# Optimization experiments

Measured on AMD Instinct MI355X. Metric: run time of the kernel, lower is better.

Reference implementation:

```python
import jax, jax.numpy as jnp
import numpy as np

NUM_LAYERS = 32
HIDDEN_DIM = 2048
RANK = 64
BATCH = 2048


def setup_inputs() -> dict:
    key = jax.random.key(0)
    k_z, k_id, k_u, k_v = jax.random.split(key, 4)
    z = jax.random.normal(k_z, (BATCH, HIDDEN_DIM), dtype=jnp.float32)
    layer_ids = jax.random.randint(k_id, (BATCH,), 0, NUM_LAYERS)
    u = jax.random.normal(k_u, (NUM_LAYERS, HIDDEN_DIM, RANK), dtype=jnp.float32) * 0.01
    v = jax.random.normal(k_v, (NUM_LAYERS, HIDDEN_DIM, RANK), dtype=jnp.float32) * 0.01
    return {"z": z, "layer_ids": layer_ids, "u": u, "v": v}


def reference(z, layer_ids, u, v):
    # Gather per-sample low-rank factors: [B, H, R]
    u_g = u[layer_ids]
    v_g = v[layer_ids]
    # proj = V_l^T z : [B, R]
    proj = jnp.einsum('bhr,bh->br', v_g, z)
    # delta = U_l proj : [B, H]
    delta = jnp.einsum('bhr,br->bh', u_g, proj)
    return z + delta
```

## Files before the change

kernel.cpp:

```cpp
#include <hip/hip_runtime.h>

#define NUM_LAYERS 32
#define HIDDEN 2048
#define RANK 64
#define BATCH 2048
#define CHK 256
#define SCP 2
#define MB 32
#define PPAD 72

typedef __attribute__((ext_vector_type(8))) short bf16x8;
typedef __attribute__((ext_vector_type(4))) float f32x4;

static __device__ __forceinline__ ushort f2bf(float x) {
    unsigned b = __builtin_bit_cast(unsigned, x);
    b += 0x7fffu + ((b >> 16) & 1u);
    return (ushort)(b >> 16);
}
static __device__ __forceinline__ ushort4 pack4(float4 v) {
    ushort4 r; r.x = f2bf(v.x); r.y = f2bf(v.y); r.z = f2bf(v.z); r.w = f2bf(v.w);
    return r;
}
static __device__ __forceinline__ bf16x8 cvt8(float4 a, float4 b) {
    bf16x8 r;
    r[0] = (short)f2bf(a.x); r[1] = (short)f2bf(a.y);
    r[2] = (short)f2bf(a.z); r[3] = (short)f2bf(a.w);
    r[4] = (short)f2bf(b.x); r[5] = (short)f2bf(b.y);
    r[6] = (short)f2bf(b.z); r[7] = (short)f2bf(b.w);
    return r;
}


__global__ __launch_bounds__(256)
void k_setup(const int* __restrict__ ids, float* __restrict__ proj,
             int* __restrict__ counts, int* __restrict__ offsets,
             int* __restrict__ perm)
{
    const int t = threadIdx.x;
    if (blockIdx.x == 0) {
        __shared__ int cnt[NUM_LAYERS];
        __shared__ int off[NUM_LAYERS];
        __shared__ int cur[NUM_LAYERS];
        if (t < NUM_LAYERS) cnt[t] = 0;
        __syncthreads();
        for (int i = t; i < BATCH; i += 256) atomicAdd(&cnt[ids[i]], 1);
        __syncthreads();
        if (t == 0) {
            int a = 0;
            for (int l = 0; l < NUM_LAYERS; ++l) { off[l] = a; a += cnt[l]; }
        }
        __syncthreads();
        if (t < NUM_LAYERS) { cur[t] = 0; counts[t] = cnt[t]; offsets[t] = off[t]; }
        __syncthreads();
        for (int i = t; i < BATCH; i += 256) {
            int l = ids[i];
            int p = off[l] + atomicAdd(&cur[l], 1);
            perm[p] = i;
        }
    } else {
        const int base = (blockIdx.x - 1) * (BATCH * RANK / 64);
        for (int i = t; i < BATCH * RANK / 64; i += 256) proj[base + i] = 0.0f;
    }
}

__global__ __launch_bounds__(256)
void k_proj(const float* __restrict__ z, const float* __restrict__ v,
            const int* __restrict__ counts, const int* __restrict__ offsets,
            const int* __restrict__ perm, float* __restrict__ proj)
{
    const int kc = blockIdx.x, l = blockIdx.y, sc = blockIdx.z;
    const int n = counts[l], o = offsets[l];
    if (sc * MB >= n) return;
    const int t = threadIdx.x;
    const int w = t >> 6, lane = t & 63;
    const int m16 = lane & 15, quad = lane >> 4;
    const int kbase = kc * CHK;

    __shared__ int bidx[MB];

    const float* vp = v + ((size_t)l * HIDDEN + kbase + quad * 8) * RANK
                    + w * 16 + m16;

    for (int base = sc * MB; base < n; base += SCP * MB) {
        const int nb = (n - base < MB) ? (n - base) : MB;
        __syncthreads();
        if (t < MB) bidx[t] = (t < nb) ? perm[o + base + t] : 0;
        __syncthreads();

        const float* zp0 = z + (size_t)bidx[m16] * HIDDEN + kbase + quad * 8;
        const float* zp1 = z + (size_t)bidx[16 + m16] * HIDDEN + kbase + quad * 8;

        f32x4 acc0 = {0.f, 0.f, 0.f, 0.f};
        f32x4 acc1 = {0.f, 0.f, 0.f, 0.f};
        #pragma unroll
        for (int kt = 0; kt < 8; ++kt) {
            float vj[8];
            #pragma unroll
            for (int j = 0; j < 8; ++j) vj[j] = vp[(size_t)(kt * 32 + j) * RANK];
            const bf16x8 bm = cvt8(make_float4(vj[0], vj[1], vj[2], vj[3]),
                                   make_float4(vj[4], vj[5], vj[6], vj[7]));
            const bf16x8 a0 = cvt8(*(const float4*)&zp0[kt * 32],
                                   *(const float4*)&zp0[kt * 32 + 4]);
            const bf16x8 a1 = cvt8(*(const float4*)&zp1[kt * 32],
                                   *(const float4*)&zp1[kt * 32 + 4]);
            acc0 = __builtin_amdgcn_mfma_f32_16x16x32_bf16(a0, bm, acc0, 0, 0, 0);
            acc1 = __builtin_amdgcn_mfma_f32_16x16x32_bf16(a1, bm, acc1, 0, 0, 0);
        }
        #pragma unroll
        for (int reg = 0; reg < 4; ++reg) {
            const int row = quad * 4 + reg;
            if (row < nb)
                atomicAdd(&proj[(size_t)bidx[row] * RANK + w * 16 + m16], acc0[reg]);
            if (16 + row < nb)
                atomicAdd(&proj[(size_t)bidx[16 + row] * RANK + w * 16 + m16], acc1[reg]);
        }
    }
}

__global__ __launch_bounds__(256)
void k_delta(const float* __restrict__ z, const float* __restrict__ u,
             const int* __restrict__ counts, const int* __restrict__ offsets,
             const int* __restrict__ perm, const float* __restrict__ proj,
             float* __restrict__ out)
{
    const int hc = blockIdx.x, l = blockIdx.y, sc = blockIdx.z;
    const int n = counts[l], o = offsets[l];
    if (sc * MB >= n) return;
    const int t = threadIdx.x;
    const int w = t >> 6, lane = t & 63;
    const int m16 = lane & 15, quad = lane >> 4;
    const int hbase = hc * CHK;

    __shared__ ushort pt[MB * PPAD];
    __shared__ int bidx[MB];

    const float* ub = u + ((size_t)l * HIDDEN + hbase) * RANK;

    for (int base = sc * MB; base < n; base += SCP * MB) {
        const int nb = (n - base < MB) ? (n - base) : MB;
        __syncthreads();
        if (t < MB) bidx[t] = (t < nb) ? perm[o + base + t] : 0;
        __syncthreads();
        #pragma unroll
        for (int it = 0; it < 2; ++it) {
            const int idx = it * 256 + t;
            const int si = idx >> 4, rq = idx & 15;
            const float4 f = *(const float4*)&proj[(size_t)bidx[si] * RANK + rq * 4];
            *(ushort4*)&pt[si * PPAD + rq * 4] = pack4(f);
        }
        __syncthreads();

        const bf16x8 pa0 = *(const bf16x8*)&pt[m16 * PPAD + quad * 8];
        const bf16x8 pa1 = *(const bf16x8*)&pt[m16 * PPAD + 32 + quad * 8];
        const bf16x8 pb0 = *(const bf16x8*)&pt[(16 + m16) * PPAD + quad * 8];
        const bf16x8 pb1 = *(const bf16x8*)&pt[(16 + m16) * PPAD + 32 + quad * 8];

        f32x4 acc0[4], acc1[4];
        #pragma unroll
        for (int nt = 0; nt < 4; ++nt) {
            acc0[nt] = (f32x4){0.f, 0.f, 0.f, 0.f};
            acc1[nt] = (f32x4){0.f, 0.f, 0.f, 0.f};
        }
        #pragma unroll
        for (int nt = 0; nt < 4; ++nt) {
            const int hcol = (w * 4 + nt) * 16 + m16;
            const float* ur = ub + (size_t)hcol * RANK;
            const bf16x8 b0 = cvt8(*(const float4*)&ur[quad * 8],
                                   *(const float4*)&ur[quad * 8 + 4]);
            const bf16x8 b1 = cvt8(*(const float4*)&ur[32 + quad * 8],
                                   *(const float4*)&ur[32 + quad * 8 + 4]);
            acc0[nt] = __builtin_amdgcn_mfma_f32_16x16x32_bf16(pa0, b0, acc0[nt], 0, 0, 0);
            acc0[nt] = __builtin_amdgcn_mfma_f32_16x16x32_bf16(pa1, b1, acc0[nt], 0, 0, 0);
            acc1[nt] = __builtin_amdgcn_mfma_f32_16x16x32_bf16(pb0, b0, acc1[nt], 0, 0, 0);
            acc1[nt] = __builtin_amdgcn_mfma_f32_16x16x32_bf16(pb1, b1, acc1[nt], 0, 0, 0);
        }
        #pragma unroll
        for (int reg = 0; reg < 4; ++reg) {
            const int si = quad * 4 + reg;
            if (si < nb) {
                const size_t rowb = (size_t)bidx[si] * HIDDEN + hbase;
                #pragma unroll
                for (int nt = 0; nt < 4; ++nt) {
                    const int hcol = (w * 4 + nt) * 16 + m16;
                    out[rowb + hcol] = z[rowb + hcol] + acc0[nt][reg];
                }
            }
            if (16 + si < nb) {
                const size_t rowb = (size_t)bidx[16 + si] * HIDDEN + hbase;
                #pragma unroll
                for (int nt = 0; nt < 4; ++nt) {
                    const int hcol = (w * 4 + nt) * 16 + m16;
                    out[rowb + hcol] = z[rowb + hcol] + acc1[nt][reg];
                }
            }
        }
    }
}

extern "C" void kernel_launch(void* const* d_in, const int* in_sizes, int n_in,
                              void* d_out, int out_size, void* d_ws, size_t ws_size,
                              hipStream_t stream)
{
    const float* z   = (const float*)d_in[0];
    const int*   ids = (const int*)d_in[1];
    const float* u   = (const float*)d_in[2];
    const float* v   = (const float*)d_in[3];
    float* out = (float*)d_out;

    float* proj  = (float*)d_ws;
    int* counts  = (int*)(proj + (size_t)BATCH * RANK);
    int* offsets = counts + NUM_LAYERS;
    int* perm    = offsets + NUM_LAYERS;

    hipLaunchKernelGGL(k_setup, dim3(65), dim3(256), 0, stream,
                       ids, proj, counts, offsets, perm);
    hipLaunchKernelGGL(k_proj, dim3(HIDDEN / CHK, NUM_LAYERS, SCP), dim3(256), 0, stream,
                       z, v, counts, offsets, perm, proj);
    hipLaunchKernelGGL(k_delta, dim3(HIDDEN / CHK, NUM_LAYERS, SCP), dim3(256), 0, stream,
                       z, u, counts, offsets, perm, proj, out);
}
```

Before: 115.4 us.

## Stage U/V/Z tiles in LDS as bf16 and replace atomics with per-chunk partials

The projection and delta kernels now load each block's V or U weight tile once into shared memory as bf16, instead of converting strided global loads inside every batch iteration. The z tile for the projection is also staged in LDS. Atomic accumulation into proj is replaced by per-K-chunk partial buffers that the delta kernel sums, which also removes the zeroing pass in setup. The cost is more LDS use, which may lower occupancy, plus extra partial-buffer reads in the delta kernel.

```diff
diff --git a/kernel.cpp b/kernel.cpp
--- a/kernel.cpp
+++ b/kernel.cpp
@@ -5,8 +5,12 @@
 #define RANK 64
 #define BATCH 2048
 #define CHK 256
+#define NKC (HIDDEN / CHK)
 #define SCP 2
 #define MB 32
+#define VPAD 264
+#define ZPAD 264
+#define UPAD 72
 #define PPAD 72
 
 typedef __attribute__((ext_vector_type(8))) short bf16x8;
@@ -21,52 +25,38 @@
     ushort4 r; r.x = f2bf(v.x); r.y = f2bf(v.y); r.z = f2bf(v.z); r.w = f2bf(v.w);
     return r;
 }
-static __device__ __forceinline__ bf16x8 cvt8(float4 a, float4 b) {
-    bf16x8 r;
-    r[0] = (short)f2bf(a.x); r[1] = (short)f2bf(a.y);
-    r[2] = (short)f2bf(a.z); r[3] = (short)f2bf(a.w);
-    r[4] = (short)f2bf(b.x); r[5] = (short)f2bf(b.y);
-    r[6] = (short)f2bf(b.z); r[7] = (short)f2bf(b.w);
-    return r;
-}
 
 
 __global__ __launch_bounds__(256)
-void k_setup(const int* __restrict__ ids, float* __restrict__ proj,
-             int* __restrict__ counts, int* __restrict__ offsets,
-             int* __restrict__ perm)
+void k_setup(const int* __restrict__ ids, int* __restrict__ counts,
+             int* __restrict__ offsets, int* __restrict__ perm)
 {
     const int t = threadIdx.x;
-    if (blockIdx.x == 0) {
-        __shared__ int cnt[NUM_LAYERS];
-        __shared__ int off[NUM_LAYERS];
-        __shared__ int cur[NUM_LAYERS];
-        if (t < NUM_LAYERS) cnt[t] = 0;
-        __syncthreads();
-        for (int i = t; i < BATCH; i += 256) atomicAdd(&cnt[ids[i]], 1);
-        __syncthreads();
-        if (t == 0) {
-            int a = 0;
-            for (int l = 0; l < NUM_LAYERS; ++l) { off[l] = a; a += cnt[l]; }
-        }
-        __syncthreads();
-        if (t < NUM_LAYERS) { cur[t] = 0; counts[t] = cnt[t]; offsets[t] = off[t]; }
-        __syncthreads();
-        for (int i = t; i < BATCH; i += 256) {
-            int l = ids[i];
-            int p = off[l] + atomicAdd(&cur[l], 1);
-            perm[p] = i;
-        }
-    } else {
-        const int base = (blockIdx.x - 1) * (BATCH * RANK / 64);
-        for (int i = t; i < BATCH * RANK / 64; i += 256) proj[base + i] = 0.0f;
+    __shared__ int cnt[NUM_LAYERS];
+    __shared__ int off[NUM_LAYERS];
+    __shared__ int cur[NUM_LAYERS];
+    if (t < NUM_LAYERS) cnt[t] = 0;
+    __syncthreads();
+    for (int i = t; i < BATCH; i += 256) atomicAdd(&cnt[ids[i]], 1);
+    __syncthreads();
+    if (t == 0) {
+        int a = 0;
+        for (int l = 0; l < NUM_LAYERS; ++l) { off[l] = a; a += cnt[l]; }
+    }
+    __syncthreads();
+    if (t < NUM_LAYERS) { cur[t] = 0; counts[t] = cnt[t]; offsets[t] = off[t]; }
+    __syncthreads();
+    for (int i = t; i < BATCH; i += 256) {
+        int l = ids[i];
+        int p = off[l] + atomicAdd(&cur[l], 1);
+        perm[p] = i;
     }
 }
 
 __global__ __launch_bounds__(256)
 void k_proj(const float* __restrict__ z, const float* __restrict__ v,
             const int* __restrict__ counts, const int* __restrict__ offsets,
-            const int* __restrict__ perm, float* __restrict__ proj)
+            const int* __restrict__ perm, float* __restrict__ partial)
 {
     const int kc = blockIdx.x, l = blockIdx.y, sc = blockIdx.z;
     const int n = counts[l], o = offsets[l];
@@ -76,33 +66,47 @@
     const int m16 = lane & 15, quad = lane >> 4;
     const int kbase = kc * CHK;
 
+    __shared__ ushort vt[RANK * VPAD];
+    __shared__ ushort zt[MB * ZPAD];
     __shared__ int bidx[MB];
 
-    const float* vp = v + ((size_t)l * HIDDEN + kbase + quad * 8) * RANK
-                    + w * 16 + m16;
+    #pragma unroll
+    for (int it = 0; it < 16; ++it) {
+        const int idx = it * 256 + t;
+        const int hh = idx >> 4, rq = idx & 15;
+        const float4 f = *(const float4*)
+            &v[((size_t)l * HIDDEN + kbase + hh) * RANK + rq * 4];
+        vt[(rq * 4 + 0) * VPAD + hh] = f2bf(f.x);
+        vt[(rq * 4 + 1) * VPAD + hh] = f2bf(f.y);
+        vt[(rq * 4 + 2) * VPAD + hh] = f2bf(f.z);
+        vt[(rq * 4 + 3) * VPAD + hh] = f2bf(f.w);
+    }
+
+    float* pout = partial + (size_t)kc * BATCH * RANK;
 
     for (int base = sc * MB; base < n; base += SCP * MB) {
         const int nb = (n - base < MB) ? (n - base) : MB;
         __syncthreads();
-        if (t < MB) bidx[t] = (t < nb) ? perm[o + base + t] : 0;
-        __syncthreads();
-
-        const float* zp0 = z + (size_t)bidx[m16] * HIDDEN + kbase + quad * 8;
-        const float* zp1 = z + (size_t)bidx[16 + m16] * HIDDEN + kbase + quad * 8;
+        if (t < MB) bidx[t] = (t < nb) ? perm[o + base + t] : perm[o + base];
+        __syncthreads();
+        #pragma unroll
+        for (int it = 0; it < 8; ++it) {
+            const int idx = it * 256 + t;
+            const int si = idx >> 6, q = idx & 63;
+            const float4 f = *(const float4*)
+                &z[(size_t)bidx[si] * HIDDEN + kbase + q * 4];
+            *(ushort4*)&zt[si * ZPAD + q * 4] = pack4(f);
+        }
+        __syncthreads();
 
         f32x4 acc0 = {0.f, 0.f, 0.f, 0.f};
         f32x4 acc1 = {0.f, 0.f, 0.f, 0.f};
         #pragma unroll
         for (int kt = 0; kt < 8; ++kt) {
-            float vj[8];
-            #pragma unroll
-            for (int j = 0; j < 8; ++j) vj[j] = vp[(size_t)(kt * 32 + j) * RANK];
-            const bf16x8 bm = cvt8(make_float4(vj[0], vj[1], vj[2], vj[3]),
-                                   make_float4(vj[4], vj[5], vj[6], vj[7]));
-            const bf16x8 a0 = cvt8(*(const float4*)&zp0[kt * 32],
-                                   *(const float4*)&zp0[kt * 32 + 4]);
-            const bf16x8 a1 = cvt8(*(const float4*)&zp1[kt * 32],
-                                   *(const float4*)&zp1[kt * 32 + 4]);
+            const int koff = kt * 32 + quad * 8;
+            const bf16x8 bm = *(const bf16x8*)&vt[(w * 16 + m16) * VPAD + koff];
+            const bf16x8 a0 = *(const bf16x8*)&zt[m16 * ZPAD + koff];
+            const bf16x8 a1 = *(const bf16x8*)&zt[(16 + m16) * ZPAD + koff];
             acc0 = __builtin_amdgcn_mfma_f32_16x16x32_bf16(a0, bm, acc0, 0, 0, 0);
             acc1 = __builtin_amdgcn_mfma_f32_16x16x32_bf16(a1, bm, acc1, 0, 0, 0);
         }
@@ -110,9 +114,9 @@
         for (int reg = 0; reg < 4; ++reg) {
             const int row = quad * 4 + reg;
             if (row < nb)
-                atomicAdd(&proj[(size_t)bidx[row] * RANK + w * 16 + m16], acc0[reg]);
+                pout[(size_t)bidx[row] * RANK + w * 16 + m16] = acc0[reg];
             if (16 + row < nb)
-                atomicAdd(&proj[(size_t)bidx[16 + row] * RANK + w * 16 + m16], acc1[reg]);
+                pout[(size_t)bidx[16 + row] * RANK + w * 16 + m16] = acc1[reg];
         }
     }
 }
@@ -120,7 +124,7 @@
 __global__ __launch_bounds__(256)
 void k_delta(const float* __restrict__ z, const float* __restrict__ u,
              const int* __restrict__ counts, const int* __restrict__ offsets,
-             const int* __restrict__ perm, const float* __restrict__ proj,
+             const int* __restrict__ perm, const float* __restrict__ partial,
              float* __restrict__ out)
 {
     const int hc = blockIdx.x, l = blockIdx.y, sc = blockIdx.z;
@@ -131,22 +135,36 @@
     const int m16 = lane & 15, quad = lane >> 4;
     const int hbase = hc * CHK;
 
+    __shared__ ushort ut[CHK * UPAD];
     __shared__ ushort pt[MB * PPAD];
     __shared__ int bidx[MB];
 
-    const float* ub = u + ((size_t)l * HIDDEN + hbase) * RANK;
+    #pragma unroll
+    for (int it = 0; it < 16; ++it) {
+        const int idx = it * 256 + t;
+        const int hh = idx >> 4, rq = idx & 15;
+        const float4 f = *(const float4*)
+            &u[((size_t)l * HIDDEN + hbase + hh) * RANK + rq * 4];
+        *(ushort4*)&ut[hh * UPAD + rq * 4] = pack4(f);
+    }
 
     for (int base = sc * MB; base < n; base += SCP * MB) {
         const int nb = (n - base < MB) ? (n - base) : MB;
         __syncthreads();
-        if (t < MB) bidx[t] = (t < nb) ? perm[o + base + t] : 0;
+        if (t < MB) bidx[t] = (t < nb) ? perm[o + base + t] : perm[o + base];
         __syncthreads();
         #pragma unroll
         for (int it = 0; it < 2; ++it) {
             const int idx = it * 256 + t;
             const int si = idx >> 4, rq = idx & 15;
-            const float4 f = *(const float4*)&proj[(size_t)bidx[si] * RANK + rq * 4];
-            *(ushort4*)&pt[si * PPAD + rq * 4] = pack4(f);
+            const float* pk = partial + (size_t)bidx[si] * RANK + rq * 4;
+            float4 s = *(const float4*)pk;
+            #pragma unroll
+            for (int kc = 1; kc < NKC; ++kc) {
+                const float4 p = *(const float4*)&pk[(size_t)kc * BATCH * RANK];
+                s.x += p.x; s.y += p.y; s.z += p.z; s.w += p.w;
+            }
+            *(ushort4*)&pt[si * PPAD + rq * 4] = pack4(s);
         }
         __syncthreads();
 
@@ -164,11 +182,8 @@
         #pragma unroll
         for (int nt = 0; nt < 4; ++nt) {
             const int hcol = (w * 4 + nt) * 16 + m16;
-            const float* ur = ub + (size_t)hcol * RANK;
-            const bf16x8 b0 = cvt8(*(const float4*)&ur[quad * 8],
-                                   *(const float4*)&ur[quad * 8 + 4]);
-            const bf16x8 b1 = cvt8(*(const float4*)&ur[32 + quad * 8],
-                                   *(const float4*)&ur[32 + quad * 8 + 4]);
+            const bf16x8 b0 = *(const bf16x8*)&ut[hcol * UPAD + quad * 8];
+            const bf16x8 b1 = *(const bf16x8*)&ut[hcol * UPAD + 32 + quad * 8];
             acc0[nt] = __builtin_amdgcn_mfma_f32_16x16x32_bf16(pa0, b0, acc0[nt], 0, 0, 0);
             acc0[nt] = __builtin_amdgcn_mfma_f32_16x16x32_bf16(pa1, b1, acc0[nt], 0, 0, 0);
             acc1[nt] = __builtin_amdgcn_mfma_f32_16x16x32_bf16(pb0, b0, acc1[nt], 0, 0, 0);
@@ -207,15 +222,15 @@
     const float* v   = (const float*)d_in[3];
     float* out = (float*)d_out;
 
-    float* proj  = (float*)d_ws;
-    int* counts  = (int*)(proj + (size_t)BATCH * RANK);
+    float* partial = (float*)d_ws;
+    int* counts  = (int*)(partial + (size_t)NKC * BATCH * RANK);
     int* offsets = counts + NUM_LAYERS;
     int* perm    = offsets + NUM_LAYERS;
 
-    hipLaunchKernelGGL(k_setup, dim3(65), dim3(256), 0, stream,
-                       ids, proj, counts, offsets, perm);
-    hipLaunchKernelGGL(k_proj, dim3(HIDDEN / CHK, NUM_LAYERS, SCP), dim3(256), 0, stream,
-                       z, v, counts, offsets, perm, proj);
+    hipLaunchKernelGGL(k_setup, dim3(1), dim3(256), 0, stream,
+                       ids, counts, offsets, perm);
+    hipLaunchKernelGGL(k_proj, dim3(NKC, NUM_LAYERS, SCP), dim3(256), 0, stream,
+                       z, v, counts, offsets, perm, partial);
     hipLaunchKernelGGL(k_delta, dim3(HIDDEN / CHK, NUM_LAYERS, SCP), dim3(256), 0, stream,
-                       z, u, counts, offsets, perm, proj, out);
-}
+                       z, u, counts, offsets, perm, partial, out);
+}
```

New measurement: 111.7 us. 1.03x faster.
